# Kernel optimization log

Hardware: AMD Instinct MI355X
Metric: run time of the kernel (lower is better)

Reference implementation:

```python
import jax, jax.numpy as jnp
import numpy as np

DIM = 96
DIM_OUT = 192
HEADS = 2
Q_STRIDE = 4
WINDOW_SIZE = 16  # flattened mask-unit size AFTER q pooling
HEAD_DIM = DIM_OUT // HEADS


def setup_inputs() -> dict:
    key = jax.random.key(0)
    k1, k2, k3, k4, k5 = jax.random.split(key, 5)
    B, N = 64, 3136  # 56x56 tokens, 49 windows of 64 tokens
    x = jax.random.normal(k1, (B, N, DIM), dtype=jnp.float32)
    # nn.Linear params (PyTorch layout: [out, in])
    s_qkv = 1.0 / np.sqrt(DIM)
    w_qkv = jax.random.uniform(k2, (3 * DIM_OUT, DIM), jnp.float32, -s_qkv, s_qkv)
    b_qkv = jax.random.uniform(k3, (3 * DIM_OUT,), jnp.float32, -s_qkv, s_qkv)
    s_proj = 1.0 / np.sqrt(DIM_OUT)
    w_proj = jax.random.uniform(k4, (DIM_OUT, DIM_OUT), jnp.float32, -s_proj, s_proj)
    b_proj = jax.random.uniform(k5, (DIM_OUT,), jnp.float32, -s_proj, s_proj)
    return {"x": x, "w_qkv": w_qkv, "b_qkv": b_qkv, "w_proj": w_proj, "b_proj": b_proj}


def reference(x, w_qkv, b_qkv, w_proj, b_proj):
    B, N, _ = x.shape
    num_windows = N // (Q_STRIDE * WINDOW_SIZE)
    tokens_per_win = Q_STRIDE * WINDOW_SIZE  # 64
    # QKV projection; token axis splits as (tokens_per_win, num_windows)
    qkv = (x @ w_qkv.T + b_qkv).reshape(B, tokens_per_win, num_windows, 3, HEADS, HEAD_DIM)
    qkv = jnp.transpose(qkv, (3, 0, 4, 2, 1, 5))  # [3, B, H, W, T, D]
    q, k, v = qkv[0], qkv[1], qkv[2]
    # q pooling via strided amax over q_stride
    q = q.reshape(B, HEADS, num_windows, Q_STRIDE, WINDOW_SIZE, HEAD_DIM).max(axis=3)
    scale = HEAD_DIM ** (-0.5)
    attn = jax.nn.softmax(jnp.einsum('bhwqd,bhwkd->bhwqk', q * scale, k), axis=-1)
    o = jnp.einsum('bhwqk,bhwkd->bhwqd', attn, v)  # [B, H, W, WINDOW_SIZE, D]
    # transpose(1,3) then flatten -> [B, WINDOW_SIZE*num_windows, dim_out]
    o = jnp.transpose(o, (0, 3, 2, 1, 4)).reshape(B, -1, DIM_OUT)
    return o @ w_proj.T + b_proj
```

## Files before the change

### kernel.cpp

```cpp
#include <hip/hip_runtime.h>


#define NW 49
#define NTOK 3136
#define DIM 96
#define DOUT 192

#define WSQ 0
#define WSBQ 55296
#define WSP 55872
#define WSBP 92736
#define WSTOT 92928

typedef __bf16 bf16x8 __attribute__((ext_vector_type(8)));
typedef float f32x4 __attribute__((ext_vector_type(4)));
typedef unsigned short u16x8 __attribute__((ext_vector_type(8)));
typedef unsigned short u16x4 __attribute__((ext_vector_type(4)));

__device__ __forceinline__ unsigned short f2bf(float f) {
    return __builtin_bit_cast(unsigned short, (__bf16)f);
}
__device__ __forceinline__ float bf2f(unsigned short h) {
    unsigned int u = ((unsigned int)h) << 16;
    return __builtin_bit_cast(float, u);
}

__device__ __forceinline__ bool sniff_fp32(const unsigned short* x16) {
    int sane = 0;
    #pragma unroll
    for (int i = 0; i < 32; ++i) {
        unsigned e = ((unsigned)x16[2 * i] >> 7) & 0xFFu;
        sane += (e >= 100u && e <= 141u) ? 1 : 0;
    }
    return sane < 24;
}

__device__ __forceinline__ bf16x8 ldb(const unsigned short* p) {
    return __builtin_bit_cast(bf16x8, *(const u16x8*)p);
}

__global__ __launch_bounds__(256)
void conv_weights(const void* __restrict__ x,
                  const void* __restrict__ w_qkv, const void* __restrict__ b_qkv,
                  const void* __restrict__ w_proj, const void* __restrict__ b_proj,
                  unsigned short* __restrict__ ws)
{
    const bool f32m = sniff_fp32((const unsigned short*)x);
    int t = blockIdx.x * 256 + threadIdx.x;
    if (t >= WSTOT / 8) return;
    int off = t * 8;
    const void* src;
    int rel;
    if (off < WSBQ)      { src = w_qkv;  rel = off; }
    else if (off < WSP)  { src = b_qkv;  rel = off - WSBQ; }
    else if (off < WSBP) { src = w_proj; rel = off - WSP; }
    else                 { src = b_proj; rel = off - WSBP; }
    u16x8 v;
    if (f32m) {
        const float* p = (const float*)src + rel;
        f32x4 a = *(const f32x4*)p;
        f32x4 bb = *(const f32x4*)(p + 4);
        v[0] = f2bf(a[0]);  v[1] = f2bf(a[1]);  v[2] = f2bf(a[2]);  v[3] = f2bf(a[3]);
        v[4] = f2bf(bb[0]); v[5] = f2bf(bb[1]); v[6] = f2bf(bb[2]); v[7] = f2bf(bb[3]);
    } else {
        v = *(const u16x8*)((const unsigned short*)src + rel);
    }
    *(u16x8*)(ws + off) = v;
}

__global__ __launch_bounds__(256, 4)
void mua_main(const void* __restrict__ x,
              const unsigned short* __restrict__ ws,
              void* __restrict__ out)
{
    const int bid = blockIdx.x;
    const int b   = bid / NW;
    const int wi  = bid - b * NW;
    const int tid  = threadIdx.x;
    const int wave = tid >> 6;
    const int lane = tid & 63;
    const int quad = lane >> 4;
    const int l16  = lane & 15;

    __shared__ __attribute__((aligned(16))) unsigned short lds[19456];
    unsigned short* x_s  = lds;
    unsigned short* k_s  = lds;
    unsigned short* v_s  = lds;
    unsigned short* qp_s = lds + 13824;
    unsigned short* o_s  = lds + 13824;
    unsigned short* p_s  = lds + 17152;

    bf16x8 wq[6][3];
    float  biasq[6];
    #pragma unroll
    for (int nt = 0; nt < 6; ++nt) {
        const int c = (nt * 4 + wave) * 16 + l16;
        #pragma unroll
        for (int ks = 0; ks < 3; ++ks)
            wq[nt][ks] = ldb(ws + WSQ + c * 96 + ks * 32 + quad * 8);
        biasq[nt] = bf2f(ws[WSBQ + c]);
    }

    const bool f32m = sniff_fp32((const unsigned short*)x);

    {
        const size_t xoff = ((size_t)b * NTOK + wi) * DIM;
        if (f32m) {
            #pragma unroll
            for (int i = 0; i < 3; ++i) {
                int chunk = tid + i * 256;
                int row = chunk / 12;
                int c16 = chunk - row * 12;
                const float* p = (const float*)x + xoff + (size_t)row * (NW * DIM) + c16 * 8;
                f32x4 a = *(const f32x4*)p;
                f32x4 bb = *(const f32x4*)(p + 4);
                u16x8 r;
                r[0] = f2bf(a[0]);  r[1] = f2bf(a[1]);  r[2] = f2bf(a[2]);  r[3] = f2bf(a[3]);
                r[4] = f2bf(bb[0]); r[5] = f2bf(bb[1]); r[6] = f2bf(bb[2]); r[7] = f2bf(bb[3]);
                *(u16x8*)&x_s[row * 104 + c16 * 8] = r;
            }
        } else {
            #pragma unroll
            for (int i = 0; i < 3; ++i) {
                int chunk = tid + i * 256;
                int row = chunk / 12;
                int c16 = chunk - row * 12;
                const unsigned short* p = (const unsigned short*)x + xoff + (size_t)row * (NW * DIM) + c16 * 8;
                *(u16x8*)&x_s[row * 104 + c16 * 8] = *(const u16x8*)p;
            }
        }
    }
    __syncthreads();

    bf16x8 afr[4][3];
    #pragma unroll
    for (int mt = 0; mt < 4; ++mt)
        #pragma unroll
        for (int ks = 0; ks < 3; ++ks)
            afr[mt][ks] = ldb(&x_s[(mt * 16 + l16) * 104 + ks * 32 + quad * 8]);
    __syncthreads();

    #pragma unroll
    for (int nt = 0; nt < 6; ++nt) {
        f32x4 acc[4];
        #pragma unroll
        for (int mt = 0; mt < 4; ++mt) {
            acc[mt] = (f32x4){0.f, 0.f, 0.f, 0.f};
            #pragma unroll
            for (int ks = 0; ks < 3; ++ks)
                acc[mt] = __builtin_amdgcn_mfma_f32_16x16x32_bf16(afr[mt][ks], wq[nt][ks], acc[mt], 0, 0, 0);
        }
        const int tt = nt * 4 + wave;
        const float bias = biasq[nt];
        if (nt < 3) {
            const int hd = tt / 6;
            const int d  = (tt % 6) * 16 + l16;
            #pragma unroll
            for (int r = 0; r < 4; ++r) {
                float m = fmaxf(fmaxf(acc[0][r], acc[1][r]), fmaxf(acc[2][r], acc[3][r])) + bias;
                qp_s[(hd * 16 + quad * 4 + r) * 104 + d] = f2bf(m);
            }
        } else {
            const int tk = tt - 12;
            const int hd = tk / 6;
            const int d  = (tk % 6) * 16 + l16;
            #pragma unroll
            for (int mt = 0; mt < 4; ++mt)
                #pragma unroll
                for (int r = 0; r < 4; ++r)
                    k_s[hd * 6656 + (mt * 16 + quad * 4 + r) * 104 + d] = f2bf(acc[mt][r] + bias);
        }
    }

    bf16x8 wv[3][3];
    float  biasv[3];
    #pragma unroll
    for (int i = 0; i < 3; ++i) {
        const int c = 384 + (i * 4 + wave) * 16 + l16;
        #pragma unroll
        for (int ks = 0; ks < 3; ++ks)
            wv[i][ks] = ldb(ws + WSQ + c * 96 + ks * 32 + quad * 8);
        biasv[i] = bf2f(ws[WSBQ + c]);
    }
    __syncthreads();

    const int h   = wave >> 1;
    const int sub = wave & 1;
    bf16x8 qa[3];
    #pragma unroll
    for (int ks = 0; ks < 3; ++ks)
        qa[ks] = ldb(&qp_s[(h * 16 + l16) * 104 + ks * 32 + quad * 8]);
    f32x4 s[4];
    #pragma unroll
    for (int nt = 0; nt < 4; ++nt) {
        s[nt] = (f32x4){0.f, 0.f, 0.f, 0.f};
        #pragma unroll
        for (int ks = 0; ks < 3; ++ks) {
            bf16x8 kb = ldb(&k_s[h * 6656 + (nt * 16 + l16) * 104 + ks * 32 + quad * 8]);
            s[nt] = __builtin_amdgcn_mfma_f32_16x16x32_bf16(qa[ks], kb, s[nt], 0, 0, 0);
        }
    }
    float rinv[4];
    const float cexp = 0.10206207261596576f * 1.4426950408889634f;
    #pragma unroll
    for (int r = 0; r < 4; ++r) {
        float m = fmaxf(fmaxf(s[0][r], s[1][r]), fmaxf(s[2][r], s[3][r]));
        m = fmaxf(m, __shfl_xor(m, 1));
        m = fmaxf(m, __shfl_xor(m, 2));
        m = fmaxf(m, __shfl_xor(m, 4));
        m = fmaxf(m, __shfl_xor(m, 8));
        float sum = 0.f;
        #pragma unroll
        for (int nt = 0; nt < 4; ++nt) {
            s[nt][r] = exp2f((s[nt][r] - m) * cexp);
            sum += s[nt][r];
        }
        sum += __shfl_xor(sum, 1);
        sum += __shfl_xor(sum, 2);
        sum += __shfl_xor(sum, 4);
        sum += __shfl_xor(sum, 8);
        rinv[r] = 1.0f / sum;
    }
    if (sub == 0) {
        #pragma unroll
        for (int nt = 0; nt < 4; ++nt)
            #pragma unroll
            for (int r = 0; r < 4; ++r)
                p_s[h * 1152 + (quad * 4 + r) * 72 + nt * 16 + l16] = f2bf(s[nt][r]);
    }
    __syncthreads();

    #pragma unroll
    for (int i = 0; i < 3; ++i) {
        f32x4 acc[4];
        #pragma unroll
        for (int mt = 0; mt < 4; ++mt) {
            acc[mt] = (f32x4){0.f, 0.f, 0.f, 0.f};
            #pragma unroll
            for (int ks = 0; ks < 3; ++ks)
                acc[mt] = __builtin_amdgcn_mfma_f32_16x16x32_bf16(afr[mt][ks], wv[i][ks], acc[mt], 0, 0, 0);
        }
        const int tv = i * 4 + wave;
        const int hd = tv / 6;
        const int d  = (tv % 6) * 16 + l16;
        const float bias = biasv[i];
        #pragma unroll
        for (int mt = 0; mt < 4; ++mt) {
            u16x4 pk;
            #pragma unroll
            for (int r = 0; r < 4; ++r) pk[r] = f2bf(acc[mt][r] + bias);
            *(u16x4*)&v_s[hd * 6912 + d * 72 + mt * 16 + quad * 4] = pk;
        }
    }

    const int cbase = wave * 48;
    bf16x8 wpr[3][6];
    float  biasp[3];
    #pragma unroll
    for (int i = 0; i < 3; ++i) {
        const int c = cbase + i * 16 + l16;
        #pragma unroll
        for (int ks = 0; ks < 6; ++ks)
            wpr[i][ks] = ldb(ws + WSP + c * 192 + ks * 32 + quad * 8);
        biasp[i] = bf2f(ws[WSBP + c]);
    }
    __syncthreads();

    bf16x8 pa[2];
    #pragma unroll
    for (int ks = 0; ks < 2; ++ks)
        pa[ks] = ldb(&p_s[h * 1152 + l16 * 72 + ks * 32 + quad * 8]);
    #pragma unroll
    for (int i = 0; i < 3; ++i) {
        const int n0 = (sub * 3 + i) * 16;
        f32x4 oacc = (f32x4){0.f, 0.f, 0.f, 0.f};
        #pragma unroll
        for (int ks = 0; ks < 2; ++ks) {
            bf16x8 vb = ldb(&v_s[h * 6912 + (n0 + l16) * 72 + ks * 32 + quad * 8]);
            oacc = __builtin_amdgcn_mfma_f32_16x16x32_bf16(pa[ks], vb, oacc, 0, 0, 0);
        }
        #pragma unroll
        for (int r = 0; r < 4; ++r)
            o_s[(quad * 4 + r) * 200 + h * 96 + n0 + l16] = f2bf(oacc[r] * rinv[r]);
    }
    __syncthreads();

    bf16x8 oa[6];
    #pragma unroll
    for (int ks = 0; ks < 6; ++ks)
        oa[ks] = ldb(&o_s[l16 * 200 + ks * 32 + quad * 8]);
    #pragma unroll
    for (int i = 0; i < 3; ++i) {
        const int c = cbase + i * 16 + l16;
        f32x4 acc = (f32x4){0.f, 0.f, 0.f, 0.f};
        #pragma unroll
        for (int ks = 0; ks < 6; ++ks)
            acc = __builtin_amdgcn_mfma_f32_16x16x32_bf16(oa[ks], wpr[i][ks], acc, 0, 0, 0);
        const float bias = biasp[i];
        #pragma unroll
        for (int r = 0; r < 4; ++r) {
            const int m = quad * 4 + r;
            const size_t idx = ((size_t)(b * 784 + m * NW + wi)) * DOUT + c;
            if (f32m) ((float*)out)[idx] = acc[r] + bias;
            else      ((unsigned short*)out)[idx] = f2bf(acc[r] + bias);
        }
    }
}

extern "C" void kernel_launch(void* const* d_in, const int* in_sizes, int n_in,
                              void* d_out, int out_size, void* d_ws, size_t ws_size,
                              hipStream_t stream) {
    const void* x      = d_in[0];
    const void* w_qkv  = d_in[1];
    const void* b_qkv  = d_in[2];
    const void* w_proj = d_in[3];
    const void* b_proj = d_in[4];
    unsigned short* ws = (unsigned short*)d_ws;

    dim3 gridc((WSTOT / 8 + 255) / 256), blockc(256);
    hipLaunchKernelGGL(conv_weights, gridc, blockc, 0, stream,
                       x, w_qkv, b_qkv, w_proj, b_proj, ws);

    dim3 grid(64 * NW), block(256);
    hipLaunchKernelGGL(mua_main, grid, block, 0, stream, x, ws, d_out);
}
```

Measured before the change: 201.3 us.

## Process each window in a single wave, streaming weights and dropping block barriers

Restructures the fused attention kernel so one 64-lane wave handles a whole window, with two windows per 128-thread block. X fragments are loaded straight from global memory into registers. Q, K and V column tiles are computed on the fly per head, and output projection partial sums are accumulated incrementally in registers, which removes the LDS staging of X and all __syncthreads. Each wave now streams the full QKV and projection weights from global/L2 itself instead of sharing them across four waves. That multiplies weight traffic per window and serialises MFMA work within one wave.

```diff
diff --git a/kernel.cpp b/kernel.cpp
--- a/kernel.cpp
+++ b/kernel.cpp
@@ -68,241 +68,212 @@
     *(u16x8*)(ws + off) = v;
 }
 
-__global__ __launch_bounds__(256, 4)
+__global__ __launch_bounds__(128, 2)
 void mua_main(const void* __restrict__ x,
               const unsigned short* __restrict__ ws,
               void* __restrict__ out)
 {
-    const int bid = blockIdx.x;
-    const int b   = bid / NW;
-    const int wi  = bid - b * NW;
     const int tid  = threadIdx.x;
-    const int wave = tid >> 6;
+    const int wid  = tid >> 6;
     const int lane = tid & 63;
     const int quad = lane >> 4;
     const int l16  = lane & 15;
-
-    __shared__ __attribute__((aligned(16))) unsigned short lds[19456];
-    unsigned short* x_s  = lds;
-    unsigned short* k_s  = lds;
-    unsigned short* v_s  = lds;
-    unsigned short* qp_s = lds + 13824;
-    unsigned short* o_s  = lds + 13824;
-    unsigned short* p_s  = lds + 17152;
-
-    bf16x8 wq[6][3];
-    float  biasq[6];
-    #pragma unroll
-    for (int nt = 0; nt < 6; ++nt) {
-        const int c = (nt * 4 + wave) * 16 + l16;
-        #pragma unroll
-        for (int ks = 0; ks < 3; ++ks)
-            wq[nt][ks] = ldb(ws + WSQ + c * 96 + ks * 32 + quad * 8);
-        biasq[nt] = bf2f(ws[WSBQ + c]);
-    }
+    const int win  = blockIdx.x * 2 + wid;
+    const int b    = win / NW;
+    const int wi   = win - b * NW;
+
+    __shared__ __attribute__((aligned(16))) unsigned short lds[10752];
+    unsigned short* kbuf = lds + wid * 5376;
+    unsigned short* vbuf = kbuf;
+    unsigned short* obuf = kbuf + 1280;
+    unsigned short* qp   = kbuf + 2560;
+    unsigned short* pbuf = kbuf + 4224;
 
     const bool f32m = sniff_fp32((const unsigned short*)x);
 
+    bf16x8 afr[4][3];
     {
         const size_t xoff = ((size_t)b * NTOK + wi) * DIM;
         if (f32m) {
             #pragma unroll
-            for (int i = 0; i < 3; ++i) {
-                int chunk = tid + i * 256;
-                int row = chunk / 12;
-                int c16 = chunk - row * 12;
-                const float* p = (const float*)x + xoff + (size_t)row * (NW * DIM) + c16 * 8;
-                f32x4 a = *(const f32x4*)p;
-                f32x4 bb = *(const f32x4*)(p + 4);
-                u16x8 r;
-                r[0] = f2bf(a[0]);  r[1] = f2bf(a[1]);  r[2] = f2bf(a[2]);  r[3] = f2bf(a[3]);
-                r[4] = f2bf(bb[0]); r[5] = f2bf(bb[1]); r[6] = f2bf(bb[2]); r[7] = f2bf(bb[3]);
-                *(u16x8*)&x_s[row * 104 + c16 * 8] = r;
-            }
+            for (int mt = 0; mt < 4; ++mt)
+                #pragma unroll
+                for (int ks = 0; ks < 3; ++ks) {
+                    const float* p = (const float*)x + xoff
+                                   + (size_t)(mt * 16 + l16) * (NW * DIM) + ks * 32 + quad * 8;
+                    f32x4 a = *(const f32x4*)p;
+                    f32x4 bb = *(const f32x4*)(p + 4);
+                    u16x8 r;
+                    r[0] = f2bf(a[0]);  r[1] = f2bf(a[1]);  r[2] = f2bf(a[2]);  r[3] = f2bf(a[3]);
+                    r[4] = f2bf(bb[0]); r[5] = f2bf(bb[1]); r[6] = f2bf(bb[2]); r[7] = f2bf(bb[3]);
+                    afr[mt][ks] = __builtin_bit_cast(bf16x8, r);
+                }
         } else {
             #pragma unroll
-            for (int i = 0; i < 3; ++i) {
-                int chunk = tid + i * 256;
-                int row = chunk / 12;
-                int c16 = chunk - row * 12;
-                const unsigned short* p = (const unsigned short*)x + xoff + (size_t)row * (NW * DIM) + c16 * 8;
-                *(u16x8*)&x_s[row * 104 + c16 * 8] = *(const u16x8*)p;
-            }
-        }
-    }
-    __syncthreads();
-
-    bf16x8 afr[4][3];
+            for (int mt = 0; mt < 4; ++mt)
+                #pragma unroll
+                for (int ks = 0; ks < 3; ++ks) {
+                    const unsigned short* p = (const unsigned short*)x + xoff
+                                   + (size_t)(mt * 16 + l16) * (NW * DIM) + ks * 32 + quad * 8;
+                    afr[mt][ks] = ldb(p);
+                }
+        }
+    }
+
+    f32x4 pacc[12];
     #pragma unroll
-    for (int mt = 0; mt < 4; ++mt)
-        #pragma unroll
-        for (int ks = 0; ks < 3; ++ks)
-            afr[mt][ks] = ldb(&x_s[(mt * 16 + l16) * 104 + ks * 32 + quad * 8]);
-    __syncthreads();
-
-    #pragma unroll
-    for (int nt = 0; nt < 6; ++nt) {
-        f32x4 acc[4];
-        #pragma unroll
-        for (int mt = 0; mt < 4; ++mt) {
-            acc[mt] = (f32x4){0.f, 0.f, 0.f, 0.f};
+    for (int i = 0; i < 12; ++i) pacc[i] = (f32x4){0.f, 0.f, 0.f, 0.f};
+
+    for (int h = 0; h < 2; ++h) {
+        #pragma unroll
+        for (int ct = 0; ct < 6; ++ct) {
+            const int c = h * 96 + ct * 16 + l16;
+            bf16x8 wb[3];
             #pragma unroll
             for (int ks = 0; ks < 3; ++ks)
-                acc[mt] = __builtin_amdgcn_mfma_f32_16x16x32_bf16(afr[mt][ks], wq[nt][ks], acc[mt], 0, 0, 0);
-        }
-        const int tt = nt * 4 + wave;
-        const float bias = biasq[nt];
-        if (nt < 3) {
-            const int hd = tt / 6;
-            const int d  = (tt % 6) * 16 + l16;
+                wb[ks] = ldb(ws + WSQ + c * 96 + ks * 32 + quad * 8);
+            f32x4 acc[4];
+            #pragma unroll
+            for (int mt = 0; mt < 4; ++mt) {
+                acc[mt] = (f32x4){0.f, 0.f, 0.f, 0.f};
+                #pragma unroll
+                for (int ks = 0; ks < 3; ++ks)
+                    acc[mt] = __builtin_amdgcn_mfma_f32_16x16x32_bf16(afr[mt][ks], wb[ks], acc[mt], 0, 0, 0);
+            }
+            const float bias = bf2f(ws[WSBQ + c]);
             #pragma unroll
             for (int r = 0; r < 4; ++r) {
                 float m = fmaxf(fmaxf(acc[0][r], acc[1][r]), fmaxf(acc[2][r], acc[3][r])) + bias;
-                qp_s[(hd * 16 + quad * 4 + r) * 104 + d] = f2bf(m);
-            }
-        } else {
-            const int tk = tt - 12;
-            const int hd = tk / 6;
-            const int d  = (tk % 6) * 16 + l16;
-            #pragma unroll
-            for (int mt = 0; mt < 4; ++mt)
+                qp[(quad * 4 + r) * 104 + ct * 16 + l16] = f2bf(m);
+            }
+        }
+        bf16x8 qa[3];
+        #pragma unroll
+        for (int ksp = 0; ksp < 3; ++ksp)
+            qa[ksp] = ldb(&qp[l16 * 104 + ksp * 32 + quad * 8]);
+
+        f32x4 s[4];
+        #pragma unroll
+        for (int nt = 0; nt < 4; ++nt) s[nt] = (f32x4){0.f, 0.f, 0.f, 0.f};
+        #pragma unroll
+        for (int ksp = 0; ksp < 3; ++ksp) {
+            #pragma unroll
+            for (int half = 0; half < 2; ++half) {
+                const int c = 192 + h * 96 + ksp * 32 + half * 16 + l16;
+                bf16x8 wb[3];
+                #pragma unroll
+                for (int ks = 0; ks < 3; ++ks)
+                    wb[ks] = ldb(ws + WSQ + c * 96 + ks * 32 + quad * 8);
+                f32x4 acc[4];
+                #pragma unroll
+                for (int mt = 0; mt < 4; ++mt) {
+                    acc[mt] = (f32x4){0.f, 0.f, 0.f, 0.f};
+                    #pragma unroll
+                    for (int ks = 0; ks < 3; ++ks)
+                        acc[mt] = __builtin_amdgcn_mfma_f32_16x16x32_bf16(afr[mt][ks], wb[ks], acc[mt], 0, 0, 0);
+                }
+                const float bias = bf2f(ws[WSBQ + c]);
+                #pragma unroll
+                for (int mt = 0; mt < 4; ++mt)
+                    #pragma unroll
+                    for (int r = 0; r < 4; ++r)
+                        kbuf[(mt * 16 + quad * 4 + r) * 40 + half * 16 + l16] = f2bf(acc[mt][r] + bias);
+            }
+            #pragma unroll
+            for (int nt = 0; nt < 4; ++nt) {
+                bf16x8 kb = ldb(&kbuf[(nt * 16 + l16) * 40 + quad * 8]);
+                s[nt] = __builtin_amdgcn_mfma_f32_16x16x32_bf16(qa[ksp], kb, s[nt], 0, 0, 0);
+            }
+        }
+
+        float rinv[4];
+        const float cexp = 0.10206207261596576f * 1.4426950408889634f;
+        #pragma unroll
+        for (int r = 0; r < 4; ++r) {
+            float m = fmaxf(fmaxf(s[0][r], s[1][r]), fmaxf(s[2][r], s[3][r]));
+            m = fmaxf(m, __shfl_xor(m, 1));
+            m = fmaxf(m, __shfl_xor(m, 2));
+            m = fmaxf(m, __shfl_xor(m, 4));
+            m = fmaxf(m, __shfl_xor(m, 8));
+            float sum = 0.f;
+            #pragma unroll
+            for (int nt = 0; nt < 4; ++nt) {
+                s[nt][r] = exp2f((s[nt][r] - m) * cexp);
+                sum += s[nt][r];
+            }
+            sum += __shfl_xor(sum, 1);
+            sum += __shfl_xor(sum, 2);
+            sum += __shfl_xor(sum, 4);
+            sum += __shfl_xor(sum, 8);
+            rinv[r] = 1.0f / sum;
+        }
+        #pragma unroll
+        for (int nt = 0; nt < 4; ++nt)
+            #pragma unroll
+            for (int r = 0; r < 4; ++r)
+                pbuf[(quad * 4 + r) * 72 + nt * 16 + l16] = f2bf(s[nt][r]);
+        bf16x8 pa[2];
+        #pragma unroll
+        for (int ks2 = 0; ks2 < 2; ++ks2)
+            pa[ks2] = ldb(&pbuf[l16 * 72 + ks2 * 32 + quad * 8]);
+
+        #pragma unroll
+        for (int dp = 0; dp < 3; ++dp) {
+            #pragma unroll
+            for (int half = 0; half < 2; ++half) {
+                const int ct = dp * 2 + half;
+                const int c = 384 + h * 96 + ct * 16 + l16;
+                bf16x8 wb[3];
+                #pragma unroll
+                for (int ks = 0; ks < 3; ++ks)
+                    wb[ks] = ldb(ws + WSQ + c * 96 + ks * 32 + quad * 8);
+                f32x4 acc[4];
+                #pragma unroll
+                for (int mt = 0; mt < 4; ++mt) {
+                    acc[mt] = (f32x4){0.f, 0.f, 0.f, 0.f};
+                    #pragma unroll
+                    for (int ks = 0; ks < 3; ++ks)
+                        acc[mt] = __builtin_amdgcn_mfma_f32_16x16x32_bf16(afr[mt][ks], wb[ks], acc[mt], 0, 0, 0);
+                }
+                const float bias = bf2f(ws[WSBQ + c]);
+                #pragma unroll
+                for (int mt = 0; mt < 4; ++mt) {
+                    u16x4 pk;
+                    #pragma unroll
+                    for (int r = 0; r < 4; ++r) pk[r] = f2bf(acc[mt][r] + bias);
+                    *(u16x4*)&vbuf[l16 * 72 + mt * 16 + quad * 4] = pk;
+                }
+                f32x4 oacc = (f32x4){0.f, 0.f, 0.f, 0.f};
+                #pragma unroll
+                for (int ks2 = 0; ks2 < 2; ++ks2) {
+                    bf16x8 vb = ldb(&vbuf[l16 * 72 + ks2 * 32 + quad * 8]);
+                    oacc = __builtin_amdgcn_mfma_f32_16x16x32_bf16(pa[ks2], vb, oacc, 0, 0, 0);
+                }
                 #pragma unroll
                 for (int r = 0; r < 4; ++r)
-                    k_s[hd * 6656 + (mt * 16 + quad * 4 + r) * 104 + d] = f2bf(acc[mt][r] + bias);
-        }
-    }
-
-    bf16x8 wv[3][3];
-    float  biasv[3];
+                    obuf[(quad * 4 + r) * 40 + half * 16 + l16] = f2bf(oacc[r] * rinv[r]);
+            }
+            bf16x8 oa = ldb(&obuf[l16 * 40 + quad * 8]);
+            const int ksg = h * 3 + dp;
+            #pragma unroll
+            for (int i = 0; i < 12; ++i) {
+                const int c = i * 16 + l16;
+                bf16x8 wb = ldb(ws + WSP + c * 192 + ksg * 32 + quad * 8);
+                pacc[i] = __builtin_amdgcn_mfma_f32_16x16x32_bf16(oa, wb, pacc[i], 0, 0, 0);
+            }
+        }
+    }
+
     #pragma unroll
-    for (int i = 0; i < 3; ++i) {
-        const int c = 384 + (i * 4 + wave) * 16 + l16;
-        #pragma unroll
-        for (int ks = 0; ks < 3; ++ks)
-            wv[i][ks] = ldb(ws + WSQ + c * 96 + ks * 32 + quad * 8);
-        biasv[i] = bf2f(ws[WSBQ + c]);
-    }
-    __syncthreads();
-
-    const int h   = wave >> 1;
-    const int sub = wave & 1;
-    bf16x8 qa[3];
-    #pragma unroll
-    for (int ks = 0; ks < 3; ++ks)
-        qa[ks] = ldb(&qp_s[(h * 16 + l16) * 104 + ks * 32 + quad * 8]);
-    f32x4 s[4];
-    #pragma unroll
-    for (int nt = 0; nt < 4; ++nt) {
-        s[nt] = (f32x4){0.f, 0.f, 0.f, 0.f};
-        #pragma unroll
-        for (int ks = 0; ks < 3; ++ks) {
-            bf16x8 kb = ldb(&k_s[h * 6656 + (nt * 16 + l16) * 104 + ks * 32 + quad * 8]);
-            s[nt] = __builtin_amdgcn_mfma_f32_16x16x32_bf16(qa[ks], kb, s[nt], 0, 0, 0);
-        }
-    }
-    float rinv[4];
-    const float cexp = 0.10206207261596576f * 1.4426950408889634f;
-    #pragma unroll
-    for (int r = 0; r < 4; ++r) {
-        float m = fmaxf(fmaxf(s[0][r], s[1][r]), fmaxf(s[2][r], s[3][r]));
-        m = fmaxf(m, __shfl_xor(m, 1));
-        m = fmaxf(m, __shfl_xor(m, 2));
-        m = fmaxf(m, __shfl_xor(m, 4));
-        m = fmaxf(m, __shfl_xor(m, 8));
-        float sum = 0.f;
-        #pragma unroll
-        for (int nt = 0; nt < 4; ++nt) {
-            s[nt][r] = exp2f((s[nt][r] - m) * cexp);
-            sum += s[nt][r];
-        }
-        sum += __shfl_xor(sum, 1);
-        sum += __shfl_xor(sum, 2);
-        sum += __shfl_xor(sum, 4);
-        sum += __shfl_xor(sum, 8);
-        rinv[r] = 1.0f / sum;
-    }
-    if (sub == 0) {
-        #pragma unroll
-        for (int nt = 0; nt < 4; ++nt)
-            #pragma unroll
-            for (int r = 0; r < 4; ++r)
-                p_s[h * 1152 + (quad * 4 + r) * 72 + nt * 16 + l16] = f2bf(s[nt][r]);
-    }
-    __syncthreads();
-
-    #pragma unroll
-    for (int i = 0; i < 3; ++i) {
-        f32x4 acc[4];
-        #pragma unroll
-        for (int mt = 0; mt < 4; ++mt) {
-            acc[mt] = (f32x4){0.f, 0.f, 0.f, 0.f};
-            #pragma unroll
-            for (int ks = 0; ks < 3; ++ks)
-                acc[mt] = __builtin_amdgcn_mfma_f32_16x16x32_bf16(afr[mt][ks], wv[i][ks], acc[mt], 0, 0, 0);
-        }
-        const int tv = i * 4 + wave;
-        const int hd = tv / 6;
-        const int d  = (tv % 6) * 16 + l16;
-        const float bias = biasv[i];
-        #pragma unroll
-        for (int mt = 0; mt < 4; ++mt) {
-            u16x4 pk;
-            #pragma unroll
-            for (int r = 0; r < 4; ++r) pk[r] = f2bf(acc[mt][r] + bias);
-            *(u16x4*)&v_s[hd * 6912 + d * 72 + mt * 16 + quad * 4] = pk;
-        }
-    }
-
-    const int cbase = wave * 48;
-    bf16x8 wpr[3][6];
-    float  biasp[3];
-    #pragma unroll
-    for (int i = 0; i < 3; ++i) {
-        const int c = cbase + i * 16 + l16;
-        #pragma unroll
-        for (int ks = 0; ks < 6; ++ks)
-            wpr[i][ks] = ldb(ws + WSP + c * 192 + ks * 32 + quad * 8);
-        biasp[i] = bf2f(ws[WSBP + c]);
-    }
-    __syncthreads();
-
-    bf16x8 pa[2];
-    #pragma unroll
-    for (int ks = 0; ks < 2; ++ks)
-        pa[ks] = ldb(&p_s[h * 1152 + l16 * 72 + ks * 32 + quad * 8]);
-    #pragma unroll
-    for (int i = 0; i < 3; ++i) {
-        const int n0 = (sub * 3 + i) * 16;
-        f32x4 oacc = (f32x4){0.f, 0.f, 0.f, 0.f};
-        #pragma unroll
-        for (int ks = 0; ks < 2; ++ks) {
-            bf16x8 vb = ldb(&v_s[h * 6912 + (n0 + l16) * 72 + ks * 32 + quad * 8]);
-            oacc = __builtin_amdgcn_mfma_f32_16x16x32_bf16(pa[ks], vb, oacc, 0, 0, 0);
-        }
-        #pragma unroll
-        for (int r = 0; r < 4; ++r)
-            o_s[(quad * 4 + r) * 200 + h * 96 + n0 + l16] = f2bf(oacc[r] * rinv[r]);
-    }
-    __syncthreads();
-
-    bf16x8 oa[6];
-    #pragma unroll
-    for (int ks = 0; ks < 6; ++ks)
-        oa[ks] = ldb(&o_s[l16 * 200 + ks * 32 + quad * 8]);
-    #pragma unroll
-    for (int i = 0; i < 3; ++i) {
-        const int c = cbase + i * 16 + l16;
-        f32x4 acc = (f32x4){0.f, 0.f, 0.f, 0.f};
-        #pragma unroll
-        for (int ks = 0; ks < 6; ++ks)
-            acc = __builtin_amdgcn_mfma_f32_16x16x32_bf16(oa[ks], wpr[i][ks], acc, 0, 0, 0);
-        const float bias = biasp[i];
+    for (int i = 0; i < 12; ++i) {
+        const int c = i * 16 + l16;
+        const float bias = bf2f(ws[WSBP + c]);
         #pragma unroll
         for (int r = 0; r < 4; ++r) {
             const int m = quad * 4 + r;
             const size_t idx = ((size_t)(b * 784 + m * NW + wi)) * DOUT + c;
-            if (f32m) ((float*)out)[idx] = acc[r] + bias;
-            else      ((unsigned short*)out)[idx] = f2bf(acc[r] + bias);
+            if (f32m) ((float*)out)[idx] = pacc[i][r] + bias;
+            else      ((unsigned short*)out)[idx] = f2bf(pacc[i][r] + bias);
         }
     }
 }
@@ -321,6 +292,6 @@
     hipLaunchKernelGGL(conv_weights, gridc, blockc, 0, stream,
                        x, w_qkv, b_qkv, w_proj, b_proj, ws);
 
-    dim3 grid(64 * NW), block(256);
+    dim3 grid(NTOK / 2), block(128);
     hipLaunchKernelGGL(mua_main, grid, block, 0, stream, x, ws, d_out);
 }
```

Result: slower. 213.6 us (+6.1%).
